# Optimization experiments

Measured on AMD Instinct MI355X. Metric: run time of the kernel, lower is better.

The kernel has to match this reference:

```python
import jax, jax.numpy as jnp
import numpy as np

N_NODES = 50000
N_EDGES = 800000
IN_CH = 128
OUT_CH = 128
TIME_DIM = 64


def setup_inputs() -> dict:
    key = jax.random.key(0)
    ks = jax.random.split(key, 7)
    x = jax.random.normal(ks[0], (N_NODES, IN_CH), dtype=jnp.float32)
    edge_index = jax.random.randint(ks[1], (2, N_EDGES), 0, N_NODES, dtype=jnp.int64)
    edge_t = jax.random.uniform(ks[2], (N_EDGES,), dtype=jnp.float32)
    # parameters
    freqs = jax.random.normal(ks[3], (TIME_DIM // 2,), dtype=jnp.float32)
    fan = IN_CH + TIME_DIM
    lim = float(np.sqrt(1.0 / fan))
    lin_w = jax.random.uniform(ks[4], (OUT_CH, fan), minval=-lim, maxval=lim, dtype=jnp.float32)
    lin_b = jax.random.uniform(ks[5], (OUT_CH,), minval=-lim, maxval=lim, dtype=jnp.float32)
    glim = float(np.sqrt(6.0 / (1 + OUT_CH)))
    attn = jax.random.uniform(ks[6], (1, OUT_CH), minval=-glim, maxval=glim, dtype=jnp.float32)
    return {"x": x, "edge_index": edge_index, "edge_t": edge_t,
            "freqs": freqs, "lin_w": lin_w, "lin_b": lin_b, "attn": attn}


def reference(x, edge_index, edge_t, freqs, lin_w, lin_b, attn):
    src, dst = edge_index[0], edge_index[1]
    n_nodes = x.shape[0]
    # time encoding: [E, time_dim]
    ang = edge_t[:, None] * freqs * (2.0 * jnp.pi)
    edge_attr = jnp.concatenate([jnp.sin(ang), jnp.cos(ang)], axis=-1)
    # gather source features and project: h = tanh(Linear(cat(x_j, te)))
    msg = jnp.concatenate([x[src], edge_attr], axis=-1)        # [E, in+time]
    h = jnp.tanh(msg @ lin_w.T + lin_b)                        # [E, out]
    # segment softmax over destination nodes
    alpha = (h * attn).sum(axis=-1)                            # [E]
    seg_max = jax.ops.segment_max(alpha, dst, num_segments=n_nodes)
    ex = jnp.exp(alpha - seg_max[dst])
    denom = jax.ops.segment_sum(ex, dst, num_segments=n_nodes)
    w = ex / (denom[dst] + 1e-16)
    # scatter-add aggregation
    out = jax.ops.segment_sum(h * w[:, None], dst, num_segments=n_nodes)
    return out
```

## Files before the change

kernel.cpp:

```cpp
#include <hip/hip_runtime.h>
#include <hip/hip_bf16.h>
#include <math.h>

#define IN_CHN 128
#define OUT_CHN 128
#define KD 192
#define TM 64

typedef __bf16 bf16x8 __attribute__((ext_vector_type(8)));
typedef float f32x4 __attribute__((ext_vector_type(4)));

static __device__ __forceinline__ unsigned short f2b(float f) {
    return __builtin_bit_cast(unsigned short, (__bf16)f);
}
static __device__ __forceinline__ float b2f(unsigned short b) {
    return __uint_as_float(((unsigned int)b) << 16);
}
static __device__ __forceinline__ float fast_tanh(float x) {
    float e = __expf(2.0f * x);
    return 1.0f - 2.0f * __builtin_amdgcn_rcpf(e + 1.0f);
}

#define GLL16(gsrc, ldst) \
    __builtin_amdgcn_global_load_lds( \
        (const __attribute__((address_space(1))) unsigned int*)(gsrc), \
        (__attribute__((address_space(3))) unsigned int*)(ldst), 16, 0, 0)

#define LDS_BARRIER() do { \
    asm volatile("s_waitcnt lgkmcnt(0)" ::: "memory"); \
    __builtin_amdgcn_s_barrier(); \
    __builtin_amdgcn_sched_barrier(0); \
} while (0)


__global__ __launch_bounds__(256) void cvt_x(const float* __restrict__ x,
    unsigned short* __restrict__ xb, long long n8)
{
    long long i = (long long)blockIdx.x * 256 + threadIdx.x;
    if (i >= n8) return;
    const float4* src = (const float4*)(x + i * 8);
    float4 v0 = src[0], v1 = src[1];
    ushort4 p0 = { f2b(v0.x), f2b(v0.y), f2b(v0.z), f2b(v0.w) };
    ushort4 p1 = { f2b(v1.x), f2b(v1.y), f2b(v1.z), f2b(v1.w) };
    *(ushort4*)(xb + i * 8)     = p0;
    *(ushort4*)(xb + i * 8 + 4) = p1;
}


__global__ __launch_bounds__(256) void count_deg(const int* __restrict__ ei,
                                                 int* __restrict__ deg, int E) {
    int e = blockIdx.x * 256 + threadIdx.x;
    if (e < E) atomicAdd(&deg[ei[E + e]], 1);
}

static __device__ __forceinline__ int wave_incl_scan(int v, int lane) {
    #pragma unroll
    for (int off = 1; off < 64; off <<= 1) {
        int t = __shfl_up(v, off);
        if (lane >= off) v += t;
    }
    return v;
}

__global__ __launch_bounds__(256) void scan_local(const int* __restrict__ deg,
    int* __restrict__ offs, int* __restrict__ partial, int Nn)
{
    __shared__ int wsum[4];
    int tid = threadIdx.x, lane = tid & 63, wid = tid >> 6;
    int i = blockIdx.x * 256 + tid;
    int v = (i < Nn) ? deg[i] : 0;
    int incl = wave_incl_scan(v, lane);
    if (lane == 63) wsum[wid] = incl;
    __syncthreads();
    int wpre = 0;
    for (int w = 0; w < wid; ++w) wpre += wsum[w];
    if (i < Nn) offs[i] = wpre + incl - v;
    if (tid == 255) partial[blockIdx.x] = wpre + incl;
}

__global__ __launch_bounds__(256) void scan_partial(int* __restrict__ partial, int nparts)
{
    __shared__ int wsum[4];
    int tid = threadIdx.x, lane = tid & 63, wid = tid >> 6;
    int v = (tid < nparts) ? partial[tid] : 0;
    int incl = wave_incl_scan(v, lane);
    if (lane == 63) wsum[wid] = incl;
    __syncthreads();
    int wpre = 0;
    for (int w = 0; w < wid; ++w) wpre += wsum[w];
    if (tid < nparts) partial[tid] = wpre + incl - v;
}

__global__ __launch_bounds__(256) void finalize_offs(int* __restrict__ offs,
    const int* __restrict__ partial, int* __restrict__ cursor, int Nn)
{
    int i = blockIdx.x * 256 + threadIdx.x;
    if (i < Nn) { int o = offs[i] + partial[i >> 8]; offs[i] = o; cursor[i] = o; }
}

__global__ __launch_bounds__(256) void fill_perm(const int* __restrict__ ei,
    const float* __restrict__ et, int* __restrict__ cursor,
    uint2* __restrict__ mt, int E)
{
    int e = blockIdx.x * 256 + threadIdx.x;
    if (e < E) {
        int d = ei[E + e];
        int pos = atomicAdd(&cursor[d], 1);
        mt[pos] = make_uint2((unsigned)ei[e], __float_as_uint(et[e]));
    }
}


__device__ __forceinline__ void load_meta(const uint2* __restrict__ mt,
    int tile, int E, int wv, int g, int lane, int sv[4], float& tsv)
{
    int e0 = tile * TM;
    #pragma unroll
    for (int i = 0; i < 4; ++i) {
        int e = e0 + wv * 16 + i * 4 + g;
        sv[i] = (int)mt[e < E ? e : E - 1].x;
    }
    int el = e0 + lane;
    tsv = __uint_as_float(mt[el < E ? el : E - 1].y);
}

__global__ __launch_bounds__(256) void gemm_mfma(
    const unsigned short* __restrict__ xb, const uint2* __restrict__ mt,
    const float* __restrict__ freqs, const float* __restrict__ lw,
    const float* __restrict__ lb, const float* __restrict__ attn,
    unsigned short* __restrict__ h_p, float* __restrict__ alpha4,
    int E, int Ep, int n_tiles)
{
    __shared__ unsigned short xs[2][TM][128];
    __shared__ unsigned short te[TM * 64];

    const int tid  = threadIdx.x;
    const int lane = tid & 63;
    const int wv   = tid >> 6;
    const int c16  = lane & 15;
    const int g    = lane >> 4;
    const int wbase = wv * 32;
    const int sgr  = lane & 7;

    bf16x8 Wf[6][2];
    #pragma unroll
    for (int kk = 0; kk < 6; ++kk)
        #pragma unroll
        for (int nf = 0; nf < 2; ++nf) {
            const float* wp = lw + (size_t)(wbase + nf * 16 + c16) * KD + kk * 32 + g * 8;
            float4 v0 = *(const float4*)wp;
            float4 v1 = *(const float4*)(wp + 4);
            bf16x8 b;
            b[0] = (__bf16)v0.x; b[1] = (__bf16)v0.y; b[2] = (__bf16)v0.z; b[3] = (__bf16)v0.w;
            b[4] = (__bf16)v1.x; b[5] = (__bf16)v1.y; b[6] = (__bf16)v1.z; b[7] = (__bf16)v1.w;
            Wf[kk][nf] = b;
        }

    f32x4 bias_v[2], attn_v[2];
    #pragma unroll
    for (int nf = 0; nf < 2; ++nf) {
        bias_v[nf] = *(const f32x4*)(lb   + wbase + nf * 16 + g * 4);
        attn_v[nf] = *(const f32x4*)(attn + wbase + nf * 16 + g * 4);
    }

    float frv[8];
    #pragma unroll
    for (int j = 0; j < 8; ++j) frv[j] = freqs[wv * 8 + j] * 6.283185307179586f;

    const int stride = gridDim.x;
    float ts_cur, ts_nxt;
    int sv_nxt[4];

    {
        int sv0[4];
        load_meta(mt, blockIdx.x, E, wv, g, lane, sv0, ts_cur);
        #pragma unroll
        for (int i = 0; i < 4; ++i) {
            const int rlo = i * 4 + g;
            const unsigned short* gsrc = xb + (size_t)sv0[i] * IN_CHN + ((c16 ^ rlo) * 8);
            GLL16(gsrc, &xs[0][wv * 16 + i * 4][0]);
        }
        int t1 = blockIdx.x + stride;
        load_meta(mt, t1 < n_tiles ? t1 : n_tiles - 1, E, wv, g, lane, sv_nxt, ts_nxt);
    }

    int cur = 0;

    for (int tile = blockIdx.x; tile < n_tiles; tile += stride) {
        const int e0 = tile * TM;

        ushort4 tp[4];
        {
            float sj[8], cj[8];
            #pragma unroll
            for (int j = 0; j < 8; ++j) {
                float ang = ts_cur * frv[j];
                sj[j] = __sinf(ang);
                cj[j] = __cosf(ang);
            }
            tp[0] = (ushort4){ f2b(sj[0]), f2b(sj[1]), f2b(sj[2]), f2b(sj[3]) };
            tp[1] = (ushort4){ f2b(sj[4]), f2b(sj[5]), f2b(sj[6]), f2b(sj[7]) };
            tp[2] = (ushort4){ f2b(cj[0]), f2b(cj[1]), f2b(cj[2]), f2b(cj[3]) };
            tp[3] = (ushort4){ f2b(cj[4]), f2b(cj[5]), f2b(cj[6]), f2b(cj[7]) };
        }

        int sv2[4]; float ts2;
        {
            int t2 = tile + 2 * stride;
            load_meta(mt, t2 < n_tiles ? t2 : n_tiles - 1, E, wv, g, lane, sv2, ts2);
        }

        __syncthreads();

        if (tile + stride < n_tiles) {
            #pragma unroll
            for (int i = 0; i < 4; ++i) {
                const int rlo = i * 4 + g;
                const unsigned short* gsrc = xb + (size_t)sv_nxt[i] * IN_CHN + ((c16 ^ rlo) * 8);
                GLL16(gsrc, &xs[cur ^ 1][wv * 16 + i * 4][0]);
            }
        }

        {
            unsigned short* tr = &te[lane * 64];
            int gs = (wv ^ sgr) * 8;
            int gc = ((wv + 4) ^ sgr) * 8;
            *(ushort4*)(tr + gs)     = tp[0];
            *(ushort4*)(tr + gs + 4) = tp[1];
            *(ushort4*)(tr + gc)     = tp[2];
            *(ushort4*)(tr + gc + 4) = tp[3];
        }

        LDS_BARRIER();

        f32x4 acc[4][2];
        #pragma unroll
        for (int mi = 0; mi < 4; ++mi) {
            acc[mi][0] = (f32x4){0.f, 0.f, 0.f, 0.f};
            acc[mi][1] = (f32x4){0.f, 0.f, 0.f, 0.f};
        }

        const unsigned short* xsc = &xs[cur][0][0];
        #pragma unroll
        for (int mi = 0; mi < 4; ++mi) {
            const int r = mi * 16 + c16;
            const unsigned short* xrow = xsc + r * 128;
            #pragma unroll
            for (int kk = 0; kk < 4; ++kk) {
                const int slot = ((kk << 2) + g) ^ c16;
                bf16x8 a = __builtin_bit_cast(bf16x8, *(const uint4*)(xrow + slot * 8));
                acc[mi][0] = __builtin_amdgcn_mfma_f32_16x16x32_bf16(Wf[kk][0], a, acc[mi][0], 0, 0, 0);
                acc[mi][1] = __builtin_amdgcn_mfma_f32_16x16x32_bf16(Wf[kk][1], a, acc[mi][1], 0, 0, 0);
            }
            const unsigned short* trow = &te[r * 64];
            bf16x8 s8 = __builtin_bit_cast(bf16x8, *(const uint4*)(trow + ((g ^ (r & 7)) * 8)));
            bf16x8 c8 = __builtin_bit_cast(bf16x8, *(const uint4*)(trow + (((g + 4) ^ (r & 7)) * 8)));
            acc[mi][0] = __builtin_amdgcn_mfma_f32_16x16x32_bf16(Wf[4][0], s8, acc[mi][0], 0, 0, 0);
            acc[mi][1] = __builtin_amdgcn_mfma_f32_16x16x32_bf16(Wf[4][1], s8, acc[mi][1], 0, 0, 0);
            acc[mi][0] = __builtin_amdgcn_mfma_f32_16x16x32_bf16(Wf[5][0], c8, acc[mi][0], 0, 0, 0);
            acc[mi][1] = __builtin_amdgcn_mfma_f32_16x16x32_bf16(Wf[5][1], c8, acc[mi][1], 0, 0, 0);
        }

        #pragma unroll
        for (int mi = 0; mi < 4; ++mi) {
            int e = e0 + mi * 16 + c16;
            float p = 0.0f;
            ushort4 pv[2];
            #pragma unroll
            for (int nf = 0; nf < 2; ++nf) {
                f32x4 z = acc[mi][nf];
                #pragma unroll
                for (int r = 0; r < 4; ++r) {
                    float h = fast_tanh(z[r] + bias_v[nf][r]);
                    z[r] = h;
                    p = fmaf(h, attn_v[nf][r], p);
                }
                pv[nf] = (ushort4){ f2b(z[0]), f2b(z[1]), f2b(z[2]), f2b(z[3]) };
            }
            p += __shfl_xor(p, 16);
            p += __shfl_xor(p, 32);
            if (e < E) {
                unsigned short* hp = h_p + (size_t)e * OUT_CHN + wbase + g * 4;
                *(ushort4*)hp        = pv[0];
                *(ushort4*)(hp + 16) = pv[1];
                if (g == 0) alpha4[(size_t)wv * Ep + e] = p;
            }
        }

        ts_cur = ts_nxt; ts_nxt = ts2;
        #pragma unroll
        for (int i = 0; i < 4; ++i) sv_nxt[i] = sv2[i];
        cur ^= 1;
    }
}


__global__ __launch_bounds__(256) void sum_alpha(const float* __restrict__ a4,
    float* __restrict__ ap, int E, int Ep)
{
    int i = blockIdx.x * 256 + threadIdx.x;
    int e = i * 4;
    if (e + 3 < E) {
        float4 v0 = *(const float4*)(a4 + e);
        float4 v1 = *(const float4*)(a4 + Ep + e);
        float4 v2 = *(const float4*)(a4 + 2 * (size_t)Ep + e);
        float4 v3 = *(const float4*)(a4 + 3 * (size_t)Ep + e);
        float4 r = { v0.x + v1.x + v2.x + v3.x, v0.y + v1.y + v2.y + v3.y,
                     v0.z + v1.z + v2.z + v3.z, v0.w + v1.w + v2.w + v3.w };
        *(float4*)(ap + e) = r;
    } else {
        for (int q = e; q < E; ++q)
            ap[q] = a4[q] + a4[Ep + q] + a4[2 * (size_t)Ep + q] + a4[3 * (size_t)Ep + q];
    }
}


__global__ __launch_bounds__(256) void agg(
    const unsigned short* __restrict__ h_p, const float* __restrict__ alpha_p,
    const int* __restrict__ offs, const int* __restrict__ deg,
    float* __restrict__ out, int Nn)
{
    int wid  = threadIdx.x >> 6;
    int lane = threadIdx.x & 63;
    int node = blockIdx.x * 4 + wid;
    if (node >= Nn) return;
    int start = offs[node];
    int d = deg[node];
    int sub = lane >> 4;
    int ch  = (lane & 15) * 8;
    float4* op = (float4*)(out + (size_t)node * OUT_CHN + ch);
    if (d == 0) {
        if (sub == 0) { op[0] = (float4){0,0,0,0}; op[1] = (float4){0,0,0,0}; }
        return;
    }

    float m = -INFINITY;
    for (int i = lane; i < d; i += 64) m = fmaxf(m, alpha_p[start + i]);
    #pragma unroll
    for (int off = 32; off > 0; off >>= 1) m = fmaxf(m, __shfl_xor(m, off));

    float s = 0.0f;
    for (int i = lane; i < d; i += 64) s += __expf(alpha_p[start + i] - m);
    #pragma unroll
    for (int off = 32; off > 0; off >>= 1) s += __shfl_xor(s, off);
    float rs = __builtin_amdgcn_rcpf(s + 1e-16f);

    float a[8];
    #pragma unroll
    for (int q = 0; q < 8; ++q) a[q] = 0.0f;

    for (int i = 0; i < d; i += 4) {
        int idx = i + sub;
        float w = 0.0f;
        uint4 hv = {0u, 0u, 0u, 0u};
        if (idx < d) {
            w = __expf(alpha_p[start + idx] - m) * rs;
            hv = *(const uint4*)(h_p + (size_t)(start + idx) * OUT_CHN + ch);
        }
        unsigned int hw[4] = { hv.x, hv.y, hv.z, hv.w };
        #pragma unroll
        for (int q = 0; q < 4; ++q) {
            a[2*q]   = fmaf(b2f((unsigned short)(hw[q] & 0xFFFFu)), w, a[2*q]);
            a[2*q+1] = fmaf(b2f((unsigned short)(hw[q] >> 16)),     w, a[2*q+1]);
        }
    }
    #pragma unroll
    for (int q = 0; q < 8; ++q) {
        a[q] += __shfl_xor(a[q], 16);
        a[q] += __shfl_xor(a[q], 32);
    }
    if (sub == 0) {
        op[0] = (float4){a[0], a[1], a[2], a[3]};
        op[1] = (float4){a[4], a[5], a[6], a[7]};
    }
}


extern "C" void kernel_launch(void* const* d_in, const int* in_sizes, int n_in,
                              void* d_out, int out_size, void* d_ws, size_t ws_size,
                              hipStream_t stream) {
    const float* x     = (const float*)d_in[0];
    const int*   ei    = (const int*)d_in[1];
    const float* et    = (const float*)d_in[2];
    const float* freqs = (const float*)d_in[3];
    const float* lw    = (const float*)d_in[4];
    const float* lb    = (const float*)d_in[5];
    const float* attn  = (const float*)d_in[6];
    float* out = (float*)d_out;

    const int E  = in_sizes[2];
    const int Nn = in_sizes[0] / IN_CHN;
    const int Ep = (E + 3) & ~3;

    char* ws = (char*)d_ws;
    unsigned short* h_p = (unsigned short*)ws;
    size_t off = (size_t)E * OUT_CHN * sizeof(unsigned short);
    float* alpha_p = (float*)(ws + off); off += (size_t)Ep * sizeof(float);
    float* alpha4  = (float*)(ws + off); off += (size_t)Ep * 4 * sizeof(float);
    uint2* mt      = (uint2*)(ws + off); off += (size_t)E * sizeof(uint2);
    unsigned short* xb = (unsigned short*)(ws + off); off += (size_t)Nn * IN_CHN * sizeof(unsigned short);
    int*   deg     = (int*)(ws + off);   off += (size_t)Nn * sizeof(int);
    int*   offs    = (int*)(ws + off);   off += (size_t)Nn * sizeof(int);
    int*   cursor  = (int*)(ws + off);   off += (size_t)Nn * sizeof(int);
    int*   partial = (int*)(ws + off);

    const int nblk = (Nn + 255) / 256;
    const int eblk = (E + 255) / 256;

    long long n8 = (long long)Nn * IN_CHN / 8;
    cvt_x<<<(unsigned)((n8 + 255) / 256), 256, 0, stream>>>(x, xb, n8);

    hipMemsetAsync(deg, 0, (size_t)Nn * sizeof(int), stream);
    count_deg<<<eblk, 256, 0, stream>>>(ei, deg, E);
    scan_local<<<nblk, 256, 0, stream>>>(deg, offs, partial, Nn);
    scan_partial<<<1, 256, 0, stream>>>(partial, nblk);
    finalize_offs<<<nblk, 256, 0, stream>>>(offs, partial, cursor, Nn);
    fill_perm<<<eblk, 256, 0, stream>>>(ei, et, cursor, mt, E);

    const int n_tiles = (E + TM - 1) / TM;
    gemm_mfma<<<1024, 256, 0, stream>>>(xb, mt, freqs, lw, lb, attn,
                                        h_p, alpha4, E, Ep, n_tiles);

    sum_alpha<<<(Ep / 4 + 255) / 256, 256, 0, stream>>>(alpha4, alpha_p, E, Ep);

    agg<<<(Nn + 3) / 4, 256, 0, stream>>>(h_p, alpha_p, offs, deg, out, Nn);
}
```

Baseline: 250.8 us.

## Halve GEMM tile rows for occupancy and drop segment-max pass in softmax

The edge GEMM tile shrinks from 64 to 32 rows. Registers and LDS per block drop, so the kernel declares a minimum of 5 blocks per CU, the grid grows to 1280 blocks, and the MFMA section runs at raised wave priority. The time encoding is spread over all 256 threads, and cosine is computed as sine with a pi/2 phase offset. The alpha-sum kernel now writes exp(alpha) directly, so the aggregation kernel no longer needs its segment-max pass; this relies on alpha staying bounded because h comes from tanh and attn is small, which trades numerical headroom for less memory traffic.

```diff
diff --git a/kernel.cpp b/kernel.cpp
--- a/kernel.cpp
+++ b/kernel.cpp
@@ -5,7 +5,7 @@
 #define IN_CHN 128
 #define OUT_CHN 128
 #define KD 192
-#define TM 64
+#define TM 32
 
 typedef __bf16 bf16x8 __attribute__((ext_vector_type(8)));
 typedef float f32x4 __attribute__((ext_vector_type(4)));
@@ -112,19 +112,19 @@
 
 
 __device__ __forceinline__ void load_meta(const uint2* __restrict__ mt,
-    int tile, int E, int wv, int g, int lane, int sv[4], float& tsv)
+    int tile, int E, int rbase, int g, int trow, int sv[2], float& tsv)
 {
     int e0 = tile * TM;
     #pragma unroll
-    for (int i = 0; i < 4; ++i) {
-        int e = e0 + wv * 16 + i * 4 + g;
+    for (int i = 0; i < 2; ++i) {
+        int e = e0 + rbase + i * 4 + g;
         sv[i] = (int)mt[e < E ? e : E - 1].x;
     }
-    int el = e0 + lane;
+    int el = e0 + trow;
     tsv = __uint_as_float(mt[el < E ? el : E - 1].y);
 }
 
-__global__ __launch_bounds__(256) void gemm_mfma(
+__global__ __launch_bounds__(256, 5) void gemm_mfma(
     const unsigned short* __restrict__ xb, const uint2* __restrict__ mt,
     const float* __restrict__ freqs, const float* __restrict__ lw,
     const float* __restrict__ lb, const float* __restrict__ attn,
@@ -140,7 +140,9 @@
     const int c16  = lane & 15;
     const int g    = lane >> 4;
     const int wbase = wv * 32;
-    const int sgr  = lane & 7;
+    const int rbase = wv * 8;
+    const int trow = tid >> 3;
+    const int tpart = tid & 7;
 
     bf16x8 Wf[6][2];
     #pragma unroll
@@ -163,25 +165,26 @@
         attn_v[nf] = *(const f32x4*)(attn + wbase + nf * 16 + g * 4);
     }
 
+    const float coff = (tpart >= 4) ? 1.5707963267948966f : 0.0f;
     float frv[8];
     #pragma unroll
-    for (int j = 0; j < 8; ++j) frv[j] = freqs[wv * 8 + j] * 6.283185307179586f;
+    for (int j = 0; j < 8; ++j) frv[j] = freqs[(tpart & 3) * 8 + j] * 6.283185307179586f;
 
     const int stride = gridDim.x;
     float ts_cur, ts_nxt;
-    int sv_nxt[4];
+    int sv_nxt[2];
 
     {
-        int sv0[4];
-        load_meta(mt, blockIdx.x, E, wv, g, lane, sv0, ts_cur);
-        #pragma unroll
-        for (int i = 0; i < 4; ++i) {
-            const int rlo = i * 4 + g;
+        int sv0[2];
+        load_meta(mt, blockIdx.x, E, rbase, g, trow, sv0, ts_cur);
+        #pragma unroll
+        for (int i = 0; i < 2; ++i) {
+            const int rlo = (rbase + i * 4 + g) & 15;
             const unsigned short* gsrc = xb + (size_t)sv0[i] * IN_CHN + ((c16 ^ rlo) * 8);
-            GLL16(gsrc, &xs[0][wv * 16 + i * 4][0]);
+            GLL16(gsrc, &xs[0][rbase + i * 4][0]);
         }
         int t1 = blockIdx.x + stride;
-        load_meta(mt, t1 < n_tiles ? t1 : n_tiles - 1, E, wv, g, lane, sv_nxt, ts_nxt);
+        load_meta(mt, t1 < n_tiles ? t1 : n_tiles - 1, E, rbase, g, trow, sv_nxt, ts_nxt);
     }
 
     int cur = 0;
@@ -189,60 +192,53 @@
     for (int tile = blockIdx.x; tile < n_tiles; tile += stride) {
         const int e0 = tile * TM;
 
-        ushort4 tp[4];
+        ushort4 tp[2];
         {
-            float sj[8], cj[8];
+            float v[8];
             #pragma unroll
-            for (int j = 0; j < 8; ++j) {
-                float ang = ts_cur * frv[j];
-                sj[j] = __sinf(ang);
-                cj[j] = __cosf(ang);
-            }
-            tp[0] = (ushort4){ f2b(sj[0]), f2b(sj[1]), f2b(sj[2]), f2b(sj[3]) };
-            tp[1] = (ushort4){ f2b(sj[4]), f2b(sj[5]), f2b(sj[6]), f2b(sj[7]) };
-            tp[2] = (ushort4){ f2b(cj[0]), f2b(cj[1]), f2b(cj[2]), f2b(cj[3]) };
-            tp[3] = (ushort4){ f2b(cj[4]), f2b(cj[5]), f2b(cj[6]), f2b(cj[7]) };
-        }
-
-        int sv2[4]; float ts2;
+            for (int j = 0; j < 8; ++j)
+                v[j] = __sinf(ts_cur * frv[j] + coff);
+            tp[0] = (ushort4){ f2b(v[0]), f2b(v[1]), f2b(v[2]), f2b(v[3]) };
+            tp[1] = (ushort4){ f2b(v[4]), f2b(v[5]), f2b(v[6]), f2b(v[7]) };
+        }
+
+        int sv2[2]; float ts2;
         {
             int t2 = tile + 2 * stride;
-            load_meta(mt, t2 < n_tiles ? t2 : n_tiles - 1, E, wv, g, lane, sv2, ts2);
+            load_meta(mt, t2 < n_tiles ? t2 : n_tiles - 1, E, rbase, g, trow, sv2, ts2);
         }
 
         __syncthreads();
 
         if (tile + stride < n_tiles) {
             #pragma unroll
-            for (int i = 0; i < 4; ++i) {
-                const int rlo = i * 4 + g;
+            for (int i = 0; i < 2; ++i) {
+                const int rlo = (rbase + i * 4 + g) & 15;
                 const unsigned short* gsrc = xb + (size_t)sv_nxt[i] * IN_CHN + ((c16 ^ rlo) * 8);
-                GLL16(gsrc, &xs[cur ^ 1][wv * 16 + i * 4][0]);
+                GLL16(gsrc, &xs[cur ^ 1][rbase + i * 4][0]);
             }
         }
 
         {
-            unsigned short* tr = &te[lane * 64];
-            int gs = (wv ^ sgr) * 8;
-            int gc = ((wv + 4) ^ sgr) * 8;
-            *(ushort4*)(tr + gs)     = tp[0];
-            *(ushort4*)(tr + gs + 4) = tp[1];
-            *(ushort4*)(tr + gc)     = tp[2];
-            *(ushort4*)(tr + gc + 4) = tp[3];
+            unsigned short* tr = &te[trow * 64];
+            int slot = (tpart ^ (trow & 7)) * 8;
+            *(ushort4*)(tr + slot)     = tp[0];
+            *(ushort4*)(tr + slot + 4) = tp[1];
         }
 
         LDS_BARRIER();
 
-        f32x4 acc[4][2];
-        #pragma unroll
-        for (int mi = 0; mi < 4; ++mi) {
+        f32x4 acc[2][2];
+        #pragma unroll
+        for (int mi = 0; mi < 2; ++mi) {
             acc[mi][0] = (f32x4){0.f, 0.f, 0.f, 0.f};
             acc[mi][1] = (f32x4){0.f, 0.f, 0.f, 0.f};
         }
 
+        __builtin_amdgcn_s_setprio(1);
         const unsigned short* xsc = &xs[cur][0][0];
         #pragma unroll
-        for (int mi = 0; mi < 4; ++mi) {
+        for (int mi = 0; mi < 2; ++mi) {
             const int r = mi * 16 + c16;
             const unsigned short* xrow = xsc + r * 128;
             #pragma unroll
@@ -252,17 +248,18 @@
                 acc[mi][0] = __builtin_amdgcn_mfma_f32_16x16x32_bf16(Wf[kk][0], a, acc[mi][0], 0, 0, 0);
                 acc[mi][1] = __builtin_amdgcn_mfma_f32_16x16x32_bf16(Wf[kk][1], a, acc[mi][1], 0, 0, 0);
             }
-            const unsigned short* trow = &te[r * 64];
-            bf16x8 s8 = __builtin_bit_cast(bf16x8, *(const uint4*)(trow + ((g ^ (r & 7)) * 8)));
-            bf16x8 c8 = __builtin_bit_cast(bf16x8, *(const uint4*)(trow + (((g + 4) ^ (r & 7)) * 8)));
+            const unsigned short* trw = &te[r * 64];
+            bf16x8 s8 = __builtin_bit_cast(bf16x8, *(const uint4*)(trw + ((g ^ (r & 7)) * 8)));
+            bf16x8 c8 = __builtin_bit_cast(bf16x8, *(const uint4*)(trw + (((g + 4) ^ (r & 7)) * 8)));
             acc[mi][0] = __builtin_amdgcn_mfma_f32_16x16x32_bf16(Wf[4][0], s8, acc[mi][0], 0, 0, 0);
             acc[mi][1] = __builtin_amdgcn_mfma_f32_16x16x32_bf16(Wf[4][1], s8, acc[mi][1], 0, 0, 0);
             acc[mi][0] = __builtin_amdgcn_mfma_f32_16x16x32_bf16(Wf[5][0], c8, acc[mi][0], 0, 0, 0);
             acc[mi][1] = __builtin_amdgcn_mfma_f32_16x16x32_bf16(Wf[5][1], c8, acc[mi][1], 0, 0, 0);
         }
-
-        #pragma unroll
-        for (int mi = 0; mi < 4; ++mi) {
+        __builtin_amdgcn_s_setprio(0);
+
+        #pragma unroll
+        for (int mi = 0; mi < 2; ++mi) {
             int e = e0 + mi * 16 + c16;
             float p = 0.0f;
             ushort4 pv[2];
@@ -288,15 +285,14 @@
         }
 
         ts_cur = ts_nxt; ts_nxt = ts2;
-        #pragma unroll
-        for (int i = 0; i < 4; ++i) sv_nxt[i] = sv2[i];
+        sv_nxt[0] = sv2[0]; sv_nxt[1] = sv2[1];
         cur ^= 1;
     }
 }
 
 
-__global__ __launch_bounds__(256) void sum_alpha(const float* __restrict__ a4,
-    float* __restrict__ ap, int E, int Ep)
+__global__ __launch_bounds__(256) void calc_ex(const float* __restrict__ a4,
+    float* __restrict__ ex, int E, int Ep)
 {
     int i = blockIdx.x * 256 + threadIdx.x;
     int e = i * 4;
@@ -305,18 +301,20 @@
         float4 v1 = *(const float4*)(a4 + Ep + e);
         float4 v2 = *(const float4*)(a4 + 2 * (size_t)Ep + e);
         float4 v3 = *(const float4*)(a4 + 3 * (size_t)Ep + e);
-        float4 r = { v0.x + v1.x + v2.x + v3.x, v0.y + v1.y + v2.y + v3.y,
-                     v0.z + v1.z + v2.z + v3.z, v0.w + v1.w + v2.w + v3.w };
-        *(float4*)(ap + e) = r;
+        float4 r = { __expf(v0.x + v1.x + v2.x + v3.x),
+                     __expf(v0.y + v1.y + v2.y + v3.y),
+                     __expf(v0.z + v1.z + v2.z + v3.z),
+                     __expf(v0.w + v1.w + v2.w + v3.w) };
+        *(float4*)(ex + e) = r;
     } else {
         for (int q = e; q < E; ++q)
-            ap[q] = a4[q] + a4[Ep + q] + a4[2 * (size_t)Ep + q] + a4[3 * (size_t)Ep + q];
+            ex[q] = __expf(a4[q] + a4[Ep + q] + a4[2 * (size_t)Ep + q] + a4[3 * (size_t)Ep + q]);
     }
 }
 
 
 __global__ __launch_bounds__(256) void agg(
-    const unsigned short* __restrict__ h_p, const float* __restrict__ alpha_p,
+    const unsigned short* __restrict__ h_p, const float* __restrict__ ex,
     const int* __restrict__ offs, const int* __restrict__ deg,
     float* __restrict__ out, int Nn)
 {
@@ -334,13 +332,8 @@
         return;
     }
 
-    float m = -INFINITY;
-    for (int i = lane; i < d; i += 64) m = fmaxf(m, alpha_p[start + i]);
-    #pragma unroll
-    for (int off = 32; off > 0; off >>= 1) m = fmaxf(m, __shfl_xor(m, off));
-
     float s = 0.0f;
-    for (int i = lane; i < d; i += 64) s += __expf(alpha_p[start + i] - m);
+    for (int i = lane; i < d; i += 64) s += ex[start + i];
     #pragma unroll
     for (int off = 32; off > 0; off >>= 1) s += __shfl_xor(s, off);
     float rs = __builtin_amdgcn_rcpf(s + 1e-16f);
@@ -354,7 +347,7 @@
         float w = 0.0f;
         uint4 hv = {0u, 0u, 0u, 0u};
         if (idx < d) {
-            w = __expf(alpha_p[start + idx] - m) * rs;
+            w = ex[start + idx] * rs;
             hv = *(const uint4*)(h_p + (size_t)(start + idx) * OUT_CHN + ch);
         }
         unsigned int hw[4] = { hv.x, hv.y, hv.z, hv.w };
@@ -395,7 +388,7 @@
     char* ws = (char*)d_ws;
     unsigned short* h_p = (unsigned short*)ws;
     size_t off = (size_t)E * OUT_CHN * sizeof(unsigned short);
-    float* alpha_p = (float*)(ws + off); off += (size_t)Ep * sizeof(float);
+    float* ex      = (float*)(ws + off); off += (size_t)Ep * sizeof(float);
     float* alpha4  = (float*)(ws + off); off += (size_t)Ep * 4 * sizeof(float);
     uint2* mt      = (uint2*)(ws + off); off += (size_t)E * sizeof(uint2);
     unsigned short* xb = (unsigned short*)(ws + off); off += (size_t)Nn * IN_CHN * sizeof(unsigned short);
@@ -418,10 +411,10 @@
     fill_perm<<<eblk, 256, 0, stream>>>(ei, et, cursor, mt, E);
 
     const int n_tiles = (E + TM - 1) / TM;
-    gemm_mfma<<<1024, 256, 0, stream>>>(xb, mt, freqs, lw, lb, attn,
+    gemm_mfma<<<1280, 256, 0, stream>>>(xb, mt, freqs, lw, lb, attn,
                                         h_p, alpha4, E, Ep, n_tiles);
 
-    sum_alpha<<<(Ep / 4 + 255) / 256, 256, 0, stream>>>(alpha4, alpha_p, E, Ep);
-
-    agg<<<(Nn + 3) / 4, 256, 0, stream>>>(h_p, alpha_p, offs, deg, out, Nn);
-}
+    calc_ex<<<(Ep / 4 + 255) / 256, 256, 0, stream>>>(alpha4, ex, E, Ep);
+
+    agg<<<(Nn + 3) / 4, 256, 0, stream>>>(h_p, ex, offs, deg, out, Nn);
+}
```

After: 512.4 us. 2.04x slower.
